# Kernel tuning notes

Hardware: AMD Instinct MI355X
Metric: run time of the kernel (lower is better)

Reference implementation:

```python
import jax, jax.numpy as jnp
import numpy as np

N_FFT = 2048
STRIDE = 512
PAD = N_FFT // 2  # center padding removed at the end
B = 4
T = 512  # number of spectrogram frames


def _make_kernels():
    n = np.arange(N_FFT)
    # ang[out_sample, freq_bin] = 2*pi*n*k/N  (create_fourier_kernels, freq_scale='no', freq_bins=n_fft)
    ang = 2.0 * np.pi * np.outer(n, n) / N_FFT
    kernel_cos = np.cos(ang).astype(np.float32)
    kernel_sin = np.sin(ang).astype(np.float32)
    # scipy.signal.get_window('hann', N, fftbins=True) -> periodic hann
    window = (0.5 - 0.5 * np.cos(2.0 * np.pi * n / N_FFT)).astype(np.float32)
    return kernel_cos, kernel_sin, window


def setup_inputs() -> dict:
    key = jax.random.key(0)
    X = jax.random.normal(key, (B, N_FFT, T, 2), dtype=jnp.float32)
    kc, ks, w = _make_kernels()
    return {
        "X": X,
        "kernel_cos": jnp.asarray(kc),
        "kernel_sin": jnp.asarray(ks),
        "window": jnp.asarray(w),
    }


def reference(X, kernel_cos, kernel_sin, window):
    # X: (B, n_fft, T, 2) complex spectrogram (onesided=False)
    b, n_fft, t, _ = X.shape
    Xr = X[..., 0]
    Xi = X[..., 1]
    # inverse DFT via dense matmul against sinusoidal kernels (conv2d in torch):
    # frames[b, n, t] = sum_f Xr[b,f,t]*cos(2pi n f/N) - Xi[b,f,t]*sin(2pi n f/N)
    frames = (jnp.einsum('bft,nf->bnt', Xr, kernel_cos)
              - jnp.einsum('bft,nf->bnt', Xi, kernel_sin))
    frames = frames * window[None, :, None] / n_fft
    # overlap-add (torch fold): out[b, t*stride + n] += frames[b, n, t]
    out_len = n_fft + STRIDE * (t - 1)
    idx = (jnp.arange(n_fft)[:, None] + STRIDE * jnp.arange(t)[None, :]).reshape(-1)
    y = jnp.zeros((b, out_len), frames.dtype).at[:, idx].add(frames.reshape(b, -1))
    # window sum-square normalization (torch_window_sumsquare)
    w_sq = jnp.broadcast_to((window * window)[:, None], (n_fft, t)).reshape(-1)
    w_sum = jnp.zeros((out_len,), window.dtype).at[idx].add(w_sq)
    nonzero = w_sum > 1e-10
    denom = jnp.where(nonzero, w_sum, jnp.ones_like(w_sum))
    y = jnp.where(nonzero[None, :], y / denom[None, :], y)
    # center=True, length=None -> trim pad_amount from both ends
    return y[:, PAD:-PAD]
```

## Files before the change

kernel.cpp:

```cpp
#include <hip/hip_runtime.h>

#define NFFT 2048
#define TT   512
#define BB   4
#define OUTL 261632
#define OUTTOT (BB*OUTL)

__device__ __forceinline__ int TIDX(int i, int c) {
    return i * 8 + ((c + i + (i >> 3)) & 7);
}

__device__ __forceinline__ float2 cmul(float2 a, float2 w) {
    return make_float2(a.x * w.x - a.y * w.y, a.x * w.y + a.y * w.x);
}

__device__ __forceinline__ void dft8(const float2 a[8], float2 o[8]) {
    float e0r = a[0].x + a[4].x, e0i = a[0].y + a[4].y;
    float e1r = a[0].x - a[4].x, e1i = a[0].y - a[4].y;
    float e2r = a[2].x + a[6].x, e2i = a[2].y + a[6].y;
    float e3r = a[6].y - a[2].y, e3i = a[2].x - a[6].x;
    float E0r = e0r + e2r, E0i = e0i + e2i;
    float E1r = e1r + e3r, E1i = e1i + e3i;
    float E2r = e0r - e2r, E2i = e0i - e2i;
    float E3r = e1r - e3r, E3i = e1i - e3i;
    float f0r = a[1].x + a[5].x, f0i = a[1].y + a[5].y;
    float f1r = a[1].x - a[5].x, f1i = a[1].y - a[5].y;
    float f2r = a[3].x + a[7].x, f2i = a[3].y + a[7].y;
    float f3r = a[7].y - a[3].y, f3i = a[3].x - a[7].x;
    float O0r = f0r + f2r, O0i = f0i + f2i;
    float O1r = f1r + f3r, O1i = f1i + f3i;
    float O2r = f0r - f2r, O2i = f0i - f2i;
    float O3r = f1r - f3r, O3i = f1i - f3i;
    const float h = 0.70710678118654752f;
    float W1r = h * (O1r - O1i), W1i = h * (O1r + O1i);
    float W2r = -O2i,            W2i = O2r;
    float W3r = -h * (O3r + O3i), W3i = h * (O3r - O3i);
    o[0] = make_float2(E0r + O0r, E0i + O0i);
    o[1] = make_float2(E1r + W1r, E1i + W1i);
    o[2] = make_float2(E2r + W2r, E2i + W2i);
    o[3] = make_float2(E3r + W3r, E3i + W3i);
    o[4] = make_float2(E0r - O0r, E0i - O0i);
    o[5] = make_float2(E1r - W1r, E1i - W1i);
    o[6] = make_float2(E2r - W2r, E2i - W2i);
    o[7] = make_float2(E3r - W3r, E3i - W3i);
}

__device__ __forceinline__ void twpow8(float2 o[8], float2 w1) {
    float2 w2 = cmul(w1, w1);
    float2 w3 = cmul(w2, w1);
    float2 w4 = cmul(w2, w2);
    o[1] = cmul(o[1], w1);
    o[2] = cmul(o[2], w2);
    o[3] = cmul(o[3], w3);
    o[4] = cmul(o[4], w4);
    o[5] = cmul(o[5], cmul(w4, w1));
    o[6] = cmul(o[6], cmul(w4, w2));
    o[7] = cmul(o[7], cmul(w4, w3));
}

__global__ __launch_bounds__(1024) void fft_k(const float* __restrict__ X,
                                              const float* __restrict__ kc,
                                              const float* __restrict__ ks,
                                              float* __restrict__ Ft) {
    __shared__ float2 tile[2048 * 8];
    __shared__ float2 tw256[256];

    const int S  = blockIdx.x;
    const int c0 = S * 8;
    const int b  = c0 >> 9;
    const int t0 = c0 & 511;
    const int tid = threadIdx.x;

    if (tid < 256)
        tw256[tid] = make_float2(kc[2048 + tid], ks[2048 + tid]);

    const float* Xb = X + ((size_t)b * 2048 * 512 + t0) * 2;
    #pragma unroll
    for (int m = 0; m < 8; m++) {
        int f = m * 256 + (tid >> 2);
        int c = (tid & 3) * 2;
        const float4 v = *reinterpret_cast<const float4*>(Xb + ((size_t)f * 512 + c) * 2);
        tile[TIDX(f, c)]     = make_float2(v.x, v.y);
        tile[TIDX(f, c + 1)] = make_float2(v.z, v.w);
    }
    __syncthreads();

    const int g = tid >> 8;
    const int u = tid & 255;
    #pragma unroll 1
    for (int r = 0; r < 2; r++) {
        const int c = r * 4 + g;
        float2 a[8], o[8];
        #pragma unroll
        for (int l = 0; l < 8; l++) a[l] = tile[TIDX(u + 256 * l, c)];
        __syncthreads();
        dft8(a, o);
        twpow8(o, tw256[u]);
        #pragma unroll
        for (int k = 0; k < 8; k++) tile[TIDX(8 * u + k, c)] = o[k];
        __syncthreads();
        #pragma unroll
        for (int l = 0; l < 8; l++) a[l] = tile[TIDX(u + 256 * l, c)];
        __syncthreads();
        dft8(a, o);
        twpow8(o, tw256[u & ~7]);
        {
            int base = 64 * (u >> 3) + (u & 7);
            #pragma unroll
            for (int k = 0; k < 8; k++) tile[TIDX(base + 8 * k, c)] = o[k];
        }
        __syncthreads();
        #pragma unroll
        for (int l = 0; l < 8; l++) a[l] = tile[TIDX(u + 256 * l, c)];
        __syncthreads();
        dft8(a, o);
        twpow8(o, tw256[u & ~63]);
        {
            int base = 512 * (u >> 6) + (u & 63);
            #pragma unroll
            for (int k = 0; k < 8; k++) tile[TIDX(base + 64 * k, c)] = o[k];
        }
        __syncthreads();
        float* outp = Ft + (size_t)(c0 + c) * 2048;
        #pragma unroll
        for (int half = 0; half < 2; half++) {
            int uu = u + 256 * half;
            float2 d0 = tile[TIDX(uu, c)];
            float2 d1 = tile[TIDX(uu + 512, c)];
            float2 d2 = tile[TIDX(uu + 1024, c)];
            float2 d3 = tile[TIDX(uu + 1536, c)];
            float p0 = d0.x + d2.x;
            float p1 = d0.x - d2.x;
            float p2 = d1.x + d3.x;
            float p3 = d3.y - d1.y;
            outp[uu]        = p0 + p2;
            outp[uu + 512]  = p1 + p3;
            outp[uu + 1024] = p0 - p2;
            outp[uu + 1536] = p1 - p3;
        }
    }
}

__global__ __launch_bounds__(256) void ola_k(const float* __restrict__ Ft,
                                             const float* __restrict__ win,
                                             float* __restrict__ out) {
    int j1 = blockIdx.x * 256 + threadIdx.x;
    if (j1 >= OUTTOT) return;
    int b  = j1 / OUTL;
    int jp = j1 - b * OUTL;
    int j  = jp + 1024;
    int tbase = j >> 9;
    int r = j & 511;
    float acc = 0.f, ws = 0.f;
    #pragma unroll
    for (int k = 0; k < 4; k++) {
        int t = tbase - k;
        if (t >= 0 && t < TT) {
            int n = r + (k << 9);
            float w = win[n];
            acc += Ft[(size_t)(b * TT + t) * NFFT + n] * w;
            ws  += w * w;
        }
    }
    float y = acc * (1.0f / (float)NFFT);
    if (ws > 1e-10f) y /= ws;
    out[j1] = y;
}

extern "C" void kernel_launch(void* const* d_in, const int* in_sizes, int n_in,
                              void* d_out, int out_size, void* d_ws, size_t ws_size,
                              hipStream_t stream) {
    const float* X  = (const float*)d_in[0];
    const float* kc = (const float*)d_in[1];
    const float* ks = (const float*)d_in[2];
    const float* w  = (const float*)d_in[3];
    float* out = (float*)d_out;

    float* Ft = (float*)d_ws;

    fft_k<<<dim3(BB * TT / 8), dim3(1024), 0, stream>>>(X, kc, ks, Ft);
    ola_k<<<dim3((OUTTOT + 255) / 256), dim3(256), 0, stream>>>(Ft, w, out);
}
```

Measured before the change: 31.63 us.

## Fuse overlap-add into FFT kernel using shared-memory frames and edge atomics

```diff
diff --git a/kernel.cpp b/kernel.cpp
--- a/kernel.cpp
+++ b/kernel.cpp
@@ -4,7 +4,6 @@
 #define TT   512
 #define BB   4
 #define OUTL 261632
-#define OUTTOT (BB*OUTL)
 
 __device__ __forceinline__ int TIDX(int i, int c) {
     return i * 8 + ((c + i + (i >> 3)) & 7);
@@ -58,10 +57,11 @@
     o[7] = cmul(o[7], cmul(w4, w3));
 }
 
-__global__ __launch_bounds__(1024) void fft_k(const float* __restrict__ X,
-                                              const float* __restrict__ kc,
-                                              const float* __restrict__ ks,
-                                              float* __restrict__ Ft) {
+__global__ __launch_bounds__(1024) void istft_k(const float* __restrict__ X,
+                                                const float* __restrict__ kc,
+                                                const float* __restrict__ ks,
+                                                const float* __restrict__ win,
+                                                float* __restrict__ out) {
     __shared__ float2 tile[2048 * 8];
     __shared__ float2 tw256[256];
 
@@ -121,7 +121,6 @@
             for (int k = 0; k < 8; k++) tile[TIDX(base + 64 * k, c)] = o[k];
         }
         __syncthreads();
-        float* outp = Ft + (size_t)(c0 + c) * 2048;
         #pragma unroll
         for (int half = 0; half < 2; half++) {
             int uu = u + 256 * half;
@@ -133,38 +132,43 @@
             float p1 = d0.x - d2.x;
             float p2 = d1.x + d3.x;
             float p3 = d3.y - d1.y;
-            outp[uu]        = p0 + p2;
-            outp[uu + 512]  = p1 + p3;
-            outp[uu + 1024] = p0 - p2;
-            outp[uu + 1536] = p1 - p3;
+            tile[TIDX(uu, c)].x        = (p0 + p2) * win[uu];
+            tile[TIDX(uu + 512, c)].x  = (p1 + p3) * win[uu + 512];
+            tile[TIDX(uu + 1024, c)].x = (p0 - p2) * win[uu + 1024];
+            tile[TIDX(uu + 1536, c)].x = (p1 - p3) * win[uu + 1536];
         }
     }
-}
+    __syncthreads();
 
-__global__ __launch_bounds__(256) void ola_k(const float* __restrict__ Ft,
-                                             const float* __restrict__ win,
-                                             float* __restrict__ out) {
-    int j1 = blockIdx.x * 256 + threadIdx.x;
-    if (j1 >= OUTTOT) return;
-    int b  = j1 / OUTL;
-    int jp = j1 - b * OUTL;
-    int j  = jp + 1024;
-    int tbase = j >> 9;
-    int r = j & 511;
-    float acc = 0.f, ws = 0.f;
     #pragma unroll
-    for (int k = 0; k < 4; k++) {
-        int t = tbase - k;
-        if (t >= 0 && t < TT) {
-            int n = r + (k << 9);
-            float w = win[n];
-            acc += Ft[(size_t)(b * TT + t) * NFFT + n] * w;
-            ws  += w * w;
+    for (int q = 0; q < 6; q++) {
+        int idx = tid + 1024 * q;
+        if (q >= 4 && idx - 4096 >= 1536) break;
+        int jl = idx;
+        int tb_l = jl >> 9;
+        int rr = jl & 511;
+        int tglob = t0 + tb_l;
+        float sum = 0.f, ws = 0.f;
+        #pragma unroll
+        for (int k = 0; k < 4; k++) {
+            int t = tglob - k;
+            int n = rr + (k << 9);
+            if (t >= 0 && t < TT) {
+                float w = win[n];
+                ws += w * w;
+                int m = tb_l - k;
+                if (m >= 0 && m < 8) sum += tile[TIDX(n, m)].x;
+            }
+        }
+        float y = sum * (1.0f / 2048.0f);
+        if (ws > 1e-10f) y /= ws;
+        int jp = t0 * 512 + jl - 1024;
+        if (jp >= 0 && jp < OUTL) {
+            float* dst = out + (size_t)b * OUTL + jp;
+            if (jl >= 1536 && jl < 4096) *dst = y;
+            else                         atomicAdd(dst, y);
         }
     }
-    float y = acc * (1.0f / (float)NFFT);
-    if (ws > 1e-10f) y /= ws;
-    out[j1] = y;
 }
 
 extern "C" void kernel_launch(void* const* d_in, const int* in_sizes, int n_in,
@@ -176,8 +180,6 @@
     const float* w  = (const float*)d_in[3];
     float* out = (float*)d_out;
 
-    float* Ft = (float*)d_ws;
-
-    fft_k<<<dim3(BB * TT / 8), dim3(1024), 0, stream>>>(X, kc, ks, Ft);
-    ola_k<<<dim3((OUTTOT + 255) / 256), dim3(256), 0, stream>>>(Ft, w, out);
+    hipMemsetAsync(out, 0, (size_t)out_size * sizeof(float), stream);
+    istft_k<<<dim3(BB * TT / 8), dim3(1024), 0, stream>>>(X, kc, ks, w, out);
 }
```

After: 32.57 us. +3.0%, slower.
